# Optimization experiments

Hardware: AMD Instinct MI355X
Metric: run time of the kernel (lower is better)

The kernel has to match this reference:

```python
import jax, jax.numpy as jnp
import numpy as np


def setup_inputs() -> dict:
    key = jax.random.key(0)
    ks = jax.random.split(key, 13)
    B, D, H, O = 4096, 2048, 3, 1  # batch, input_dim, hidden layer count, output_dim
    f32 = jnp.float32
    scale = 1.0 / np.sqrt(D)
    return {
        "x": jax.random.normal(ks[0], (B, D), f32),
        "w_mu_h": jax.random.normal(ks[1], (H, D, D), f32) * scale,
        "w_rho_h": jax.random.normal(ks[2], (H, D, D), f32) - 5.0,  # softplus(-5) ~ small std
        "b_mu_h": jax.random.normal(ks[3], (H, D), f32) * scale,
        "b_rho_h": jax.random.normal(ks[4], (H, D), f32) - 5.0,
        "w_mu_o": jax.random.normal(ks[5], (O, D), f32) * scale,
        "w_rho_o": jax.random.normal(ks[6], (O, D), f32) - 5.0,
        "b_mu_o": jax.random.normal(ks[7], (O,), f32) * scale,
        "b_rho_o": jax.random.normal(ks[8], (O,), f32) - 5.0,
        # reparameterization noise (torch.randn_like), passed explicitly for determinism
        "eps_w_h": jax.random.normal(ks[9], (H, D, D), f32),
        "eps_b_h": jax.random.normal(ks[10], (H, D), f32),
        "eps_w_o": jax.random.normal(ks[11], (O, D), f32),
        "eps_b_o": jax.random.normal(ks[12], (O,), f32),
    }


def _vlinear(x, w_mu, w_rho, b_mu, b_rho, eps_w, eps_b):
    # weight = mu + eps * softplus(rho); F.linear(x, W, b) = x @ W.T + b
    w = w_mu + eps_w * jax.nn.softplus(w_rho)
    b = b_mu + eps_b * jax.nn.softplus(b_rho)
    return x @ w.T + b


def reference(x, w_mu_h, w_rho_h, b_mu_h, b_rho_h,
              w_mu_o, w_rho_o, b_mu_o, b_rho_o,
              eps_w_h, eps_b_h, eps_w_o, eps_b_o):
    def step(h, p):
        wm, wr, bm, br, ew, eb = p
        h = jax.nn.relu(_vlinear(h, wm, wr, bm, br, ew, eb))
        return h, None

    h, _ = jax.lax.scan(step, x, (w_mu_h, w_rho_h, b_mu_h, b_rho_h, eps_w_h, eps_b_h))
    return _vlinear(h, w_mu_o, w_rho_o, b_mu_o, b_rho_o, eps_w_o, eps_b_o)
```

## Files before the change

### kernel.cpp

```cpp
#include <hip/hip_runtime.h>

#define BB 4096
#define DD 2048

typedef float f32x4 __attribute__((ext_vector_type(4)));
typedef __bf16 bf16x8 __attribute__((ext_vector_type(8)));

typedef __attribute__((address_space(1))) unsigned int gl_u32;
typedef __attribute__((address_space(3))) unsigned int lds_u32;

#define GLOAD_LDS16(gptr, sptr) \
  __builtin_amdgcn_global_load_lds((gl_u32*)(void*)(gptr), (lds_u32*)(sptr), 16, 0, 0)

__device__ __forceinline__ unsigned short f2bf(float f) {
  unsigned int u = __float_as_uint(f);
  u += 0x7fffu + ((u >> 16) & 1u);
  return (unsigned short)(u >> 16);
}

__device__ __forceinline__ float sp(float x) {
  float t = __expf(-fabsf(x));
  return fmaxf(x, 0.0f) + __logf(1.0f + t);
}

__global__ void prep_kernel(
    const float* __restrict__ x,
    const float* __restrict__ wmuh, const float* __restrict__ wrhoh,
    const float* __restrict__ bmuh, const float* __restrict__ brhoh,
    const float* __restrict__ wmuo, const float* __restrict__ wrhoo,
    const float* __restrict__ bmuo, const float* __restrict__ brhoo,
    const float* __restrict__ epswh, const float* __restrict__ epsbh,
    const float* __restrict__ epswo, const float* __restrict__ epsbo,
    unsigned short* __restrict__ Wh, unsigned short* __restrict__ Xb,
    float* __restrict__ bh, float* __restrict__ wo, float* __restrict__ bo)
{
  const long long RW = 3LL * DD * DD / 4;
  const long long RX = (long long)BB * DD / 4;
  const long long RBH = 3LL * DD / 4;
  const long long RO = DD / 4;
  long long i = (long long)blockIdx.x * 256 + threadIdx.x;
  if (i < RW) {
    float4 m = ((const float4*)wmuh)[i];
    float4 r = ((const float4*)wrhoh)[i];
    float4 e = ((const float4*)epswh)[i];
    ushort4 o;
    o.x = f2bf(m.x + e.x * sp(r.x));
    o.y = f2bf(m.y + e.y * sp(r.y));
    o.z = f2bf(m.z + e.z * sp(r.z));
    o.w = f2bf(m.w + e.w * sp(r.w));
    ((ushort4*)Wh)[i] = o;
    return;
  }
  i -= RW;
  if (i < RX) {
    float4 v = ((const float4*)x)[i];
    ushort4 o;
    o.x = f2bf(v.x); o.y = f2bf(v.y); o.z = f2bf(v.z); o.w = f2bf(v.w);
    ((ushort4*)Xb)[i] = o;
    return;
  }
  i -= RX;
  if (i < RBH) {
    float4 m = ((const float4*)bmuh)[i];
    float4 r = ((const float4*)brhoh)[i];
    float4 e = ((const float4*)epsbh)[i];
    float4 o;
    o.x = m.x + e.x * sp(r.x);
    o.y = m.y + e.y * sp(r.y);
    o.z = m.z + e.z * sp(r.z);
    o.w = m.w + e.w * sp(r.w);
    ((float4*)bh)[i] = o;
    return;
  }
  i -= RBH;
  if (i < RO) {
    float4 m = ((const float4*)wmuo)[i];
    float4 r = ((const float4*)wrhoo)[i];
    float4 e = ((const float4*)epswo)[i];
    float4 o;
    o.x = m.x + e.x * sp(r.x);
    o.y = m.y + e.y * sp(r.y);
    o.z = m.z + e.z * sp(r.z);
    o.w = m.w + e.w * sp(r.w);
    ((float4*)wo)[i] = o;
    return;
  }
  i -= RO;
  if (i == 0) {
    bo[0] = bmuo[0] + epsbo[0] * sp(brhoo[0]);
  }
}

__global__ __launch_bounds__(256) void gemm_relu_kernel(
    const unsigned short* __restrict__ A,
    const unsigned short* __restrict__ W,
    const float* __restrict__ bias,
    unsigned short* __restrict__ C,
    int N, int K)
{
  __shared__ unsigned short sA[128 * 64];
  __shared__ unsigned short sB[128 * 64];

  const int t = threadIdx.x;
  const int w = t >> 6;
  const int l = t & 63;
  const int lq = l >> 4;
  const int lr = l & 15;

  const int id = blockIdx.x;
  const int p = id & 7;
  const int i4 = id >> 3;
  const int mt = (p & 3) * 8 + (i4 & 7);
  const int nt = (p >> 2) * 8 + (i4 >> 3);
  const int m0 = mt * 128;
  const int n0 = nt * 128;

  const int mw = (w >> 1) * 64;
  const int nw = (w & 1) * 64;

  f32x4 acc[4][4] = {};

  int srow[4], sgc[4];
  #pragma unroll
  for (int i = 0; i < 4; ++i) {
    int c = i * 256 + t;
    srow[i] = c >> 3;
    sgc[i] = (c & 7) ^ (srow[i] & 7);
  }

  for (int kt = 0; kt < K; kt += 64) {
    #pragma unroll
    for (int i = 0; i < 4; ++i) {
      int c = i * 256 + t;
      const unsigned short* ga = A + (size_t)(m0 + srow[i]) * K + kt + sgc[i] * 8;
      GLOAD_LDS16(ga, &sA[c * 8]);
      const unsigned short* gb = W + (size_t)(n0 + srow[i]) * K + kt + sgc[i] * 8;
      GLOAD_LDS16(gb, &sB[c * 8]);
    }
    __syncthreads();

    #pragma unroll
    for (int s = 0; s < 2; ++s) {
      bf16x8 af[4], bfr[4];
      #pragma unroll
      for (int i = 0; i < 4; ++i) {
        int ra = mw + i * 16 + lr;
        int g = s * 4 + lq;
        af[i] = *(const bf16x8*)&sA[ra * 64 + (g ^ (ra & 7)) * 8];
        int rb = nw + i * 16 + lr;
        bfr[i] = *(const bf16x8*)&sB[rb * 64 + (g ^ (rb & 7)) * 8];
      }
      #pragma unroll
      for (int i = 0; i < 4; ++i)
        #pragma unroll
        for (int j = 0; j < 4; ++j)
          acc[i][j] = __builtin_amdgcn_mfma_f32_16x16x32_bf16(af[i], bfr[j], acc[i][j], 0, 0, 0);
    }
    __syncthreads();
  }

  #pragma unroll
  for (int j = 0; j < 4; ++j) {
    int n = n0 + nw + j * 16 + lr;
    float bv = bias[n];
    #pragma unroll
    for (int i = 0; i < 4; ++i) {
      int mbase = m0 + mw + i * 16 + lq * 4;
      #pragma unroll
      for (int r = 0; r < 4; ++r) {
        float v = acc[i][j][r] + bv;
        v = fmaxf(v, 0.0f);
        C[(size_t)(mbase + r) * N + n] = f2bf(v);
      }
    }
  }
}

__global__ void final_kernel(const unsigned short* __restrict__ H,
                             const float* __restrict__ wo,
                             const float* __restrict__ bo,
                             float* __restrict__ out)
{
  const int row = blockIdx.x * 4 + (threadIdx.x >> 6);
  const int l = threadIdx.x & 63;
  const unsigned short* hr = H + (size_t)row * DD;
  float sum = 0.0f;
  #pragma unroll
  for (int s = 0; s < 4; ++s) {
    int k = s * 512 + l * 8;
    uint4 hv = *(const uint4*)&hr[k];
    float4 w0 = *(const float4*)&wo[k];
    float4 w1 = *(const float4*)&wo[k + 4];
    sum += __uint_as_float(hv.x << 16) * w0.x;
    sum += __uint_as_float(hv.x & 0xffff0000u) * w0.y;
    sum += __uint_as_float(hv.y << 16) * w0.z;
    sum += __uint_as_float(hv.y & 0xffff0000u) * w0.w;
    sum += __uint_as_float(hv.z << 16) * w1.x;
    sum += __uint_as_float(hv.z & 0xffff0000u) * w1.y;
    sum += __uint_as_float(hv.w << 16) * w1.z;
    sum += __uint_as_float(hv.w & 0xffff0000u) * w1.w;
  }
  #pragma unroll
  for (int off = 32; off > 0; off >>= 1)
    sum += __shfl_down(sum, off, 64);
  if (l == 0) out[row] = sum + bo[0];
}

extern "C" void kernel_launch(void* const* d_in, const int* in_sizes, int n_in,
                              void* d_out, int out_size, void* d_ws, size_t ws_size,
                              hipStream_t stream) {
  const float* x     = (const float*)d_in[0];
  const float* wmuh  = (const float*)d_in[1];
  const float* wrhoh = (const float*)d_in[2];
  const float* bmuh  = (const float*)d_in[3];
  const float* brhoh = (const float*)d_in[4];
  const float* wmuo  = (const float*)d_in[5];
  const float* wrhoo = (const float*)d_in[6];
  const float* bmuo  = (const float*)d_in[7];
  const float* brhoo = (const float*)d_in[8];
  const float* epswh = (const float*)d_in[9];
  const float* epsbh = (const float*)d_in[10];
  const float* epswo = (const float*)d_in[11];
  const float* epsbo = (const float*)d_in[12];

  char* ws = (char*)d_ws;
  unsigned short* Wh = (unsigned short*)(ws);
  unsigned short* Xb = (unsigned short*)(ws + 25165824);
  unsigned short* Ha = (unsigned short*)(ws + 25165824 + 16777216);
  unsigned short* Hb = (unsigned short*)(ws + 25165824 + 2 * 16777216);
  float* bh = (float*)(ws + 25165824 + 3 * 16777216);
  float* wo = (float*)(ws + 25165824 + 3 * 16777216 + 24576);
  float* bo = (float*)(ws + 25165824 + 3 * 16777216 + 24576 + 8192);

  const int prep_blocks = (5244929 + 255) / 256;
  prep_kernel<<<prep_blocks, 256, 0, stream>>>(
      x, wmuh, wrhoh, bmuh, brhoh, wmuo, wrhoo, bmuo, brhoo,
      epswh, epsbh, epswo, epsbo, Wh, Xb, bh, wo, bo);

  const int ggrid = (BB / 128) * (DD / 128);
  gemm_relu_kernel<<<ggrid, 256, 0, stream>>>(Xb, Wh,                 bh,            Ha, DD, DD);
  gemm_relu_kernel<<<ggrid, 256, 0, stream>>>(Ha, Wh + 1 * 4194304,   bh + DD,       Hb, DD, DD);
  gemm_relu_kernel<<<ggrid, 256, 0, stream>>>(Hb, Wh + 2 * 4194304,   bh + 2 * DD,   Xb, DD, DD);

  final_kernel<<<BB / 4, 256, 0, stream>>>(Xb, wo, bo, (float*)d_out);
}
```

Before: 327.2 us.

## Use 512-thread GEMM blocks and batch four vectors per thread in prep

The GEMM block grows from 4 to 8 waves, each computing a 64x32 sub-tile instead of 64x64. This halves the accumulator registers per thread and increases waves per CU to hide load latency, at the cost of more LDS fragment reads per MFMA. The prep kernel now has each thread process four float4 elements, with all loads issued before compute, for more memory-level parallelism and fewer blocks.

```diff
diff --git a/kernel.cpp b/kernel.cpp
--- a/kernel.cpp
+++ b/kernel.cpp
@@ -34,33 +34,43 @@
     unsigned short* __restrict__ Wh, unsigned short* __restrict__ Xb,
     float* __restrict__ bh, float* __restrict__ wo, float* __restrict__ bo)
 {
-  const long long RW = 3LL * DD * DD / 4;
-  const long long RX = (long long)BB * DD / 4;
-  const long long RBH = 3LL * DD / 4;
-  const long long RO = DD / 4;
-  long long i = (long long)blockIdx.x * 256 + threadIdx.x;
-  if (i < RW) {
-    float4 m = ((const float4*)wmuh)[i];
-    float4 r = ((const float4*)wrhoh)[i];
-    float4 e = ((const float4*)epswh)[i];
-    ushort4 o;
-    o.x = f2bf(m.x + e.x * sp(r.x));
-    o.y = f2bf(m.y + e.y * sp(r.y));
-    o.z = f2bf(m.z + e.z * sp(r.z));
-    o.w = f2bf(m.w + e.w * sp(r.w));
-    ((ushort4*)Wh)[i] = o;
-    return;
-  }
-  i -= RW;
-  if (i < RX) {
-    float4 v = ((const float4*)x)[i];
-    ushort4 o;
-    o.x = f2bf(v.x); o.y = f2bf(v.y); o.z = f2bf(v.z); o.w = f2bf(v.w);
-    ((ushort4*)Xb)[i] = o;
-    return;
-  }
-  i -= RX;
-  if (i < RBH) {
+  const int b = blockIdx.x;
+  const int t = threadIdx.x;
+  if (b < 3072) {
+    long long base = (long long)b * 1024 + t;
+    float4 m[4], r[4], e[4];
+    #pragma unroll
+    for (int j = 0; j < 4; ++j) {
+      m[j] = ((const float4*)wmuh)[base + j * 256];
+      r[j] = ((const float4*)wrhoh)[base + j * 256];
+      e[j] = ((const float4*)epswh)[base + j * 256];
+    }
+    #pragma unroll
+    for (int j = 0; j < 4; ++j) {
+      ushort4 o;
+      o.x = f2bf(m[j].x + e[j].x * sp(r[j].x));
+      o.y = f2bf(m[j].y + e[j].y * sp(r[j].y));
+      o.z = f2bf(m[j].z + e[j].z * sp(r[j].z));
+      o.w = f2bf(m[j].w + e[j].w * sp(r[j].w));
+      ((ushort4*)Wh)[base + j * 256] = o;
+    }
+    return;
+  }
+  if (b < 5120) {
+    long long base = (long long)(b - 3072) * 1024 + t;
+    float4 v[4];
+    #pragma unroll
+    for (int j = 0; j < 4; ++j) v[j] = ((const float4*)x)[base + j * 256];
+    #pragma unroll
+    for (int j = 0; j < 4; ++j) {
+      ushort4 o;
+      o.x = f2bf(v[j].x); o.y = f2bf(v[j].y); o.z = f2bf(v[j].z); o.w = f2bf(v[j].w);
+      ((ushort4*)Xb)[base + j * 256] = o;
+    }
+    return;
+  }
+  long long i = (long long)(b - 5120) * 256 + t;
+  if (i < 1536) {
     float4 m = ((const float4*)bmuh)[i];
     float4 r = ((const float4*)brhoh)[i];
     float4 e = ((const float4*)epsbh)[i];
@@ -72,8 +82,8 @@
     ((float4*)bh)[i] = o;
     return;
   }
-  i -= RBH;
-  if (i < RO) {
+  i -= 1536;
+  if (i < 512) {
     float4 m = ((const float4*)wmuo)[i];
     float4 r = ((const float4*)wrhoo)[i];
     float4 e = ((const float4*)epswo)[i];
@@ -85,13 +95,13 @@
     ((float4*)wo)[i] = o;
     return;
   }
-  i -= RO;
+  i -= 512;
   if (i == 0) {
     bo[0] = bmuo[0] + epsbo[0] * sp(brhoo[0]);
   }
 }
 
-__global__ __launch_bounds__(256) void gemm_relu_kernel(
+__global__ __launch_bounds__(512) void gemm_relu_kernel(
     const unsigned short* __restrict__ A,
     const unsigned short* __restrict__ W,
     const float* __restrict__ bias,
@@ -115,23 +125,23 @@
   const int m0 = mt * 128;
   const int n0 = nt * 128;
 
-  const int mw = (w >> 1) * 64;
-  const int nw = (w & 1) * 64;
-
-  f32x4 acc[4][4] = {};
-
-  int srow[4], sgc[4];
-  #pragma unroll
-  for (int i = 0; i < 4; ++i) {
-    int c = i * 256 + t;
+  const int mw = (w >> 2) * 64;
+  const int nw = (w & 3) * 32;
+
+  f32x4 acc[4][2] = {};
+
+  int srow[2], sgc[2];
+  #pragma unroll
+  for (int i = 0; i < 2; ++i) {
+    int c = i * 512 + t;
     srow[i] = c >> 3;
     sgc[i] = (c & 7) ^ (srow[i] & 7);
   }
 
   for (int kt = 0; kt < K; kt += 64) {
     #pragma unroll
-    for (int i = 0; i < 4; ++i) {
-      int c = i * 256 + t;
+    for (int i = 0; i < 2; ++i) {
+      int c = i * 512 + t;
       const unsigned short* ga = A + (size_t)(m0 + srow[i]) * K + kt + sgc[i] * 8;
       GLOAD_LDS16(ga, &sA[c * 8]);
       const unsigned short* gb = W + (size_t)(n0 + srow[i]) * K + kt + sgc[i] * 8;
@@ -141,26 +151,29 @@
 
     #pragma unroll
     for (int s = 0; s < 2; ++s) {
-      bf16x8 af[4], bfr[4];
+      bf16x8 af[4], bfr[2];
+      int g = s * 4 + lq;
       #pragma unroll
       for (int i = 0; i < 4; ++i) {
         int ra = mw + i * 16 + lr;
-        int g = s * 4 + lq;
         af[i] = *(const bf16x8*)&sA[ra * 64 + (g ^ (ra & 7)) * 8];
-        int rb = nw + i * 16 + lr;
-        bfr[i] = *(const bf16x8*)&sB[rb * 64 + (g ^ (rb & 7)) * 8];
+      }
+      #pragma unroll
+      for (int j = 0; j < 2; ++j) {
+        int rb = nw + j * 16 + lr;
+        bfr[j] = *(const bf16x8*)&sB[rb * 64 + (g ^ (rb & 7)) * 8];
       }
       #pragma unroll
       for (int i = 0; i < 4; ++i)
         #pragma unroll
-        for (int j = 0; j < 4; ++j)
+        for (int j = 0; j < 2; ++j)
           acc[i][j] = __builtin_amdgcn_mfma_f32_16x16x32_bf16(af[i], bfr[j], acc[i][j], 0, 0, 0);
     }
     __syncthreads();
   }
 
   #pragma unroll
-  for (int j = 0; j < 4; ++j) {
+  for (int j = 0; j < 2; ++j) {
     int n = n0 + nw + j * 16 + lr;
     float bv = bias[n];
     #pragma unroll
@@ -232,15 +245,14 @@
   float* wo = (float*)(ws + 25165824 + 3 * 16777216 + 24576);
   float* bo = (float*)(ws + 25165824 + 3 * 16777216 + 24576 + 8192);
 
-  const int prep_blocks = (5244929 + 255) / 256;
-  prep_kernel<<<prep_blocks, 256, 0, stream>>>(
+  prep_kernel<<<5129, 256, 0, stream>>>(
       x, wmuh, wrhoh, bmuh, brhoh, wmuo, wrhoo, bmuo, brhoo,
       epswh, epsbh, epswo, epsbo, Wh, Xb, bh, wo, bo);
 
   const int ggrid = (BB / 128) * (DD / 128);
-  gemm_relu_kernel<<<ggrid, 256, 0, stream>>>(Xb, Wh,                 bh,            Ha, DD, DD);
-  gemm_relu_kernel<<<ggrid, 256, 0, stream>>>(Ha, Wh + 1 * 4194304,   bh + DD,       Hb, DD, DD);
-  gemm_relu_kernel<<<ggrid, 256, 0, stream>>>(Hb, Wh + 2 * 4194304,   bh + 2 * DD,   Xb, DD, DD);
+  gemm_relu_kernel<<<ggrid, 512, 0, stream>>>(Xb, Wh,               bh,          Ha, DD, DD);
+  gemm_relu_kernel<<<ggrid, 512, 0, stream>>>(Ha, Wh + 1 * 4194304, bh + DD,     Hb, DD, DD);
+  gemm_relu_kernel<<<ggrid, 512, 0, stream>>>(Hb, Wh + 2 * 4194304, bh + 2 * DD, Xb, DD, DD);
 
   final_kernel<<<BB / 4, 256, 0, stream>>>(Xb, wo, bo, (float*)d_out);
 }
```

Measured after the change: 315.9 us. 1.04x faster.
